# Optimization experiments

Hardware: AMD Instinct MI355X
Metric: run time of the kernel (lower is better)

The kernel has to match this reference:

```python
import jax, jax.numpy as jnp
import numpy as np

VOCAB = 4096
CODE_DIM = 3


def setup_inputs() -> dict:
    key = jax.random.key(0)
    k1, k2 = jax.random.split(key)
    B, L = 4, 16384
    feats = jax.random.normal(k1, (B, L, CODE_DIM), dtype=jnp.float32)
    # xavier_uniform init for the (vocab, code_dim) embedding table
    limit = float(np.sqrt(6.0 / (VOCAB + CODE_DIM)))
    codebook = jax.random.uniform(k2, (VOCAB, CODE_DIM), dtype=jnp.float32,
                                  minval=-limit, maxval=limit)
    return {"feats": feats, "codebook": codebook}


def reference(feats, codebook):
    """EMAVQ.forward (eval mode): cdist -> argmin -> gather -> vq loss -> straight-through."""
    B, L, D = feats.shape
    flat = feats.reshape(-1, D)                      # (N, D)
    dist = (jnp.sum(flat * flat, axis=1, keepdims=True)
            - 2.0 * (flat @ codebook.T)
            + jnp.sum(codebook * codebook, axis=1))  # (N, V)
    idx = jnp.argmin(dist, axis=1)                   # (N,)
    quant = codebook[idx].reshape(B, L, D)           # embedding gather
    sg = jax.lax.stop_gradient
    loss = (jnp.mean((quant - sg(feats)) ** 2)
            + 0.25 * jnp.mean((feats - sg(quant)) ** 2))
    quant_st = feats + sg(quant - feats)             # straight-through estimator
    return quant_st, idx.reshape(B, L), loss
```

## Files before the change

kernel.cpp:

```cpp
#include <hip/hip_runtime.h>

#define VOCAB 4096
#define SLICES 8
#define SLICE 512
#define GRP 8
#define NGRP (SLICE / GRP)

__device__ __forceinline__ float opaque(float x) {
  asm volatile("" : "+v"(x));
  return x;
}

__device__ __forceinline__ float min3(float a, float b, float c) {
  float d;
  asm("v_min3_f32 %0, %1, %2, %3" : "=v"(d) : "v"(a), "v"(b), "v"(c));
  return d;
}

__global__ __launch_bounds__(256) void vq_prep_kernel(
    const float* __restrict__ cb, float4* __restrict__ cw,
    float* __restrict__ loss_slot) {
  int j = blockIdx.x * 256 + threadIdx.x;
  if (j == 0) *loss_slot = 0.0f;
  if (j < VOCAB) {
    float e0 = cb[3 * j + 0];
    float e1 = cb[3 * j + 1];
    float e2 = cb[3 * j + 2];
    float p0 = opaque(e0 * e0);
    float p1 = opaque(e1 * e1);
    float p2 = opaque(e2 * e2);
    float c = opaque(opaque(p0 + p1) + p2);
    cw[j] = make_float4(e0, e1, e2, c);
  }
}

__device__ __forceinline__ float dist_f32(float x0, float x1, float x2,
                                          float a, float4 cd) {
  float m = fmaf(x2, cd.z, fmaf(x1, cd.y, x0 * cd.x));
  return fmaf(-2.0f, m, a) + cd.w;
}

__global__ __launch_bounds__(512) void vq_kernel(
    const float* __restrict__ feats, const float4* __restrict__ cw,
    float* __restrict__ out_quant, float* __restrict__ out_idx,
    float* __restrict__ out_loss, int npts) {
  __shared__ float sB[512];
  __shared__ int sI[512];
  __shared__ double sL[64];

  const int tid = threadIdx.x;
  const int lane = tid & 63;
  const int s = __builtin_amdgcn_readfirstlane(tid >> 6);
  const int p = blockIdx.x * 64 + lane;

  const float x0 = feats[3 * p + 0];
  const float x1 = feats[3 * p + 1];
  const float x2 = feats[3 * p + 2];

  float xp0 = opaque(x0 * x0);
  float xp1 = opaque(x1 * x1);
  float xp2 = opaque(x2 * x2);
  const float a = opaque(opaque(xp0 + xp1) + xp2);

  const float4* cs = cw + s * SLICE;

  float best = 3.4e38f;
  int gbase = 0;
#pragma unroll 2
  for (int g = 0; g < NGRP; ++g) {
    const float4* gp = cs + g * GRP;
    float d0 = dist_f32(x0, x1, x2, a, gp[0]);
    float d1 = dist_f32(x0, x1, x2, a, gp[1]);
    float d2 = dist_f32(x0, x1, x2, a, gp[2]);
    float d3 = dist_f32(x0, x1, x2, a, gp[3]);
    float d4 = dist_f32(x0, x1, x2, a, gp[4]);
    float d5 = dist_f32(x0, x1, x2, a, gp[5]);
    float d6 = dist_f32(x0, x1, x2, a, gp[6]);
    float d7 = dist_f32(x0, x1, x2, a, gp[7]);
    float gm = min3(min3(d0, d1, d2), min3(d3, d4, d5), fminf(d6, d7));
    if (gm < best) gbase = g;
    best = fminf(best, gm);
  }
  gbase = s * SLICE + gbase * GRP;

  sB[tid] = best;
  sI[tid] = gbase;
  __syncthreads();

  if (tid < 64) {
#pragma unroll
    for (int k = 1; k < SLICES; ++k) {
      float v = sB[tid + 64 * k];
      if (v < best) { best = v; gbase = sI[tid + 64 * k]; }
    }
    int bi = gbase;
    float bd = 3.4e38f;
    float q0 = 0.0f, q1 = 0.0f, q2 = 0.0f;
#pragma unroll
    for (int k = 0; k < GRP; ++k) {
      float4 cd = cw[gbase + k];
      float d = dist_f32(x0, x1, x2, a, cd);
      if (d < bd) { bd = d; bi = gbase + k; q0 = cd.x; q1 = cd.y; q2 = cd.z; }
    }
    float t0 = q0 - x0, t1 = q1 - x1, t2 = q2 - x2;
    out_quant[3 * p + 0] = x0 + t0;
    out_quant[3 * p + 1] = x1 + t1;
    out_quant[3 * p + 2] = x2 + t2;
    out_idx[p] = (float)bi;
    sL[tid] = (double)t0 * t0 + (double)t1 * t1 + (double)t2 * t2;
  }
  __syncthreads();

  if (tid == 0) {
    double acc = 0.0;
#pragma unroll 8
    for (int k = 0; k < 64; ++k) acc += sL[k];
    atomicAdd(out_loss, (float)(acc * (1.25 / ((double)npts * 3.0))));
  }
}

extern "C" void kernel_launch(void* const* d_in, const int* in_sizes, int n_in,
                              void* d_out, int out_size, void* d_ws,
                              size_t ws_size, hipStream_t stream) {
  const float* feats = (const float*)d_in[0];
  const float* cb = (const float*)d_in[1];
  const int npts = in_sizes[0] / 3;

  float* out = (float*)d_out;
  float* out_quant = out;
  float* out_idx = out + in_sizes[0];
  float* out_loss = out + in_sizes[0] + npts;

  float4* cw = (float4*)d_ws;

  vq_prep_kernel<<<VOCAB / 256, 256, 0, stream>>>(cb, cw, out_loss);
  vq_kernel<<<npts / 64, 512, 0, stream>>>(feats, cw, out_quant, out_idx,
                                           out_loss, npts);
}
```

Before: 107.3 us.

## Stage codebook in LDS and compute two points per thread

Each block now copies the full 4096-entry preprocessed codebook into a 64 KB shared-memory table and handles 128 points instead of 64. Each thread evaluates distances for two points against every codebook entry it reads, so each entry load serves two points and the grid is halved. The argmin refinement also reads from the shared table instead of global memory. In exchange, every block pays a 64 KB prologue load plus a barrier, and the large shared allocation limits how many blocks fit on a CU. The slice index is no longer forced wave-uniform, which may stop the compiler from using scalar broadcast loads.

```diff
diff --git a/kernel.cpp b/kernel.cpp
--- a/kernel.cpp
+++ b/kernel.cpp
@@ -5,6 +5,7 @@
 #define SLICE 512
 #define GRP 8
 #define NGRP (SLICE / GRP)
+#define PTS 128
 
 __device__ __forceinline__ float opaque(float x) {
   asm volatile("" : "+v"(x));
@@ -44,64 +45,86 @@
     const float* __restrict__ feats, const float4* __restrict__ cw,
     float* __restrict__ out_quant, float* __restrict__ out_idx,
     float* __restrict__ out_loss, int npts) {
-  __shared__ float sB[512];
-  __shared__ int sI[512];
-  __shared__ double sL[64];
+  __shared__ float4 sTab[VOCAB];
+  __shared__ float sB[SLICES * PTS];
+  __shared__ int sI[SLICES * PTS];
+  __shared__ double sL[PTS];
 
   const int tid = threadIdx.x;
   const int lane = tid & 63;
-  const int s = __builtin_amdgcn_readfirstlane(tid >> 6);
-  const int p = blockIdx.x * 64 + lane;
+  const int s = tid >> 6;
 
-  const float x0 = feats[3 * p + 0];
-  const float x1 = feats[3 * p + 1];
-  const float x2 = feats[3 * p + 2];
+#pragma unroll
+  for (int k = 0; k < VOCAB / 512; ++k) sTab[tid + k * 512] = cw[tid + k * 512];
 
-  float xp0 = opaque(x0 * x0);
-  float xp1 = opaque(x1 * x1);
-  float xp2 = opaque(x2 * x2);
-  const float a = opaque(opaque(xp0 + xp1) + xp2);
+  const int pbase = blockIdx.x * PTS;
+  const int pA = pbase + lane;
+  const int pB = pbase + 64 + lane;
 
-  const float4* cs = cw + s * SLICE;
+  const float a0 = feats[3 * pA + 0], a1 = feats[3 * pA + 1],
+              a2 = feats[3 * pA + 2];
+  const float b0 = feats[3 * pB + 0], b1 = feats[3 * pB + 1],
+              b2 = feats[3 * pB + 2];
 
-  float best = 3.4e38f;
-  int gbase = 0;
+  float ap0 = opaque(a0 * a0), ap1 = opaque(a1 * a1), ap2 = opaque(a2 * a2);
+  const float na = opaque(opaque(ap0 + ap1) + ap2);
+  float bp0 = opaque(b0 * b0), bp1 = opaque(b1 * b1), bp2 = opaque(b2 * b2);
+  const float nb = opaque(opaque(bp0 + bp1) + bp2);
+
+  __syncthreads();
+
+  const float4* cs = sTab + s * SLICE;
+
+  float bestA = 3.4e38f, bestB = 3.4e38f;
+  int gA = 0, gB = 0;
 #pragma unroll 2
   for (int g = 0; g < NGRP; ++g) {
     const float4* gp = cs + g * GRP;
-    float d0 = dist_f32(x0, x1, x2, a, gp[0]);
-    float d1 = dist_f32(x0, x1, x2, a, gp[1]);
-    float d2 = dist_f32(x0, x1, x2, a, gp[2]);
-    float d3 = dist_f32(x0, x1, x2, a, gp[3]);
-    float d4 = dist_f32(x0, x1, x2, a, gp[4]);
-    float d5 = dist_f32(x0, x1, x2, a, gp[5]);
-    float d6 = dist_f32(x0, x1, x2, a, gp[6]);
-    float d7 = dist_f32(x0, x1, x2, a, gp[7]);
-    float gm = min3(min3(d0, d1, d2), min3(d3, d4, d5), fminf(d6, d7));
-    if (gm < best) gbase = g;
-    best = fminf(best, gm);
+    float4 c0 = gp[0], c1 = gp[1], c2 = gp[2], c3 = gp[3];
+    float4 c4 = gp[4], c5 = gp[5], c6 = gp[6], c7 = gp[7];
+    float dA0 = dist_f32(a0, a1, a2, na, c0), dB0 = dist_f32(b0, b1, b2, nb, c0);
+    float dA1 = dist_f32(a0, a1, a2, na, c1), dB1 = dist_f32(b0, b1, b2, nb, c1);
+    float dA2 = dist_f32(a0, a1, a2, na, c2), dB2 = dist_f32(b0, b1, b2, nb, c2);
+    float dA3 = dist_f32(a0, a1, a2, na, c3), dB3 = dist_f32(b0, b1, b2, nb, c3);
+    float dA4 = dist_f32(a0, a1, a2, na, c4), dB4 = dist_f32(b0, b1, b2, nb, c4);
+    float dA5 = dist_f32(a0, a1, a2, na, c5), dB5 = dist_f32(b0, b1, b2, nb, c5);
+    float dA6 = dist_f32(a0, a1, a2, na, c6), dB6 = dist_f32(b0, b1, b2, nb, c6);
+    float dA7 = dist_f32(a0, a1, a2, na, c7), dB7 = dist_f32(b0, b1, b2, nb, c7);
+    float gmA = min3(min3(dA0, dA1, dA2), min3(dA3, dA4, dA5), fminf(dA6, dA7));
+    float gmB = min3(min3(dB0, dB1, dB2), min3(dB3, dB4, dB5), fminf(dB6, dB7));
+    if (gmA < bestA) gA = g;
+    bestA = fminf(bestA, gmA);
+    if (gmB < bestB) gB = g;
+    bestB = fminf(bestB, gmB);
   }
-  gbase = s * SLICE + gbase * GRP;
-
-  sB[tid] = best;
-  sI[tid] = gbase;
+  sB[s * PTS + lane] = bestA;
+  sI[s * PTS + lane] = s * SLICE + gA * GRP;
+  sB[s * PTS + 64 + lane] = bestB;
+  sI[s * PTS + 64 + lane] = s * SLICE + gB * GRP;
   __syncthreads();
 
-  if (tid < 64) {
+  if (tid < PTS) {
+    const float x0 = (s == 0) ? a0 : b0;
+    const float x1 = (s == 0) ? a1 : b1;
+    const float x2 = (s == 0) ? a2 : b2;
+    const float a = (s == 0) ? na : nb;
+    float best = sB[tid];
+    int gbase = sI[tid];
 #pragma unroll
     for (int k = 1; k < SLICES; ++k) {
-      float v = sB[tid + 64 * k];
-      if (v < best) { best = v; gbase = sI[tid + 64 * k]; }
+      float v = sB[k * PTS + tid];
+      if (v < best) { best = v; gbase = sI[k * PTS + tid]; }
     }
     int bi = gbase;
     float bd = 3.4e38f;
     float q0 = 0.0f, q1 = 0.0f, q2 = 0.0f;
 #pragma unroll
     for (int k = 0; k < GRP; ++k) {
-      float4 cd = cw[gbase + k];
+      float4 cd = sTab[gbase + k];
       float d = dist_f32(x0, x1, x2, a, cd);
       if (d < bd) { bd = d; bi = gbase + k; q0 = cd.x; q1 = cd.y; q2 = cd.z; }
     }
+    const int p = pbase + tid;
     float t0 = q0 - x0, t1 = q1 - x1, t2 = q2 - x2;
     out_quant[3 * p + 0] = x0 + t0;
     out_quant[3 * p + 1] = x1 + t1;
@@ -114,7 +137,7 @@
   if (tid == 0) {
     double acc = 0.0;
 #pragma unroll 8
-    for (int k = 0; k < 64; ++k) acc += sL[k];
+    for (int k = 0; k < PTS; ++k) acc += sL[k];
     atomicAdd(out_loss, (float)(acc * (1.25 / ((double)npts * 3.0))));
   }
 }
@@ -134,6 +157,6 @@
   float4* cw = (float4*)d_ws;
 
   vq_prep_kernel<<<VOCAB / 256, 256, 0, stream>>>(cb, cw, out_loss);
-  vq_kernel<<<npts / 64, 512, 0, stream>>>(feats, cw, out_quant, out_idx,
-                                           out_loss, npts);
+  vq_kernel<<<npts / PTS, 512, 0, stream>>>(feats, cw, out_quant, out_idx,
+                                            out_loss, npts);
 }
```

Result: faster. 94.33 us (-12.1%).
